# Optimization experiments

Hardware: AMD Instinct MI355X
Metric: run time of the kernel (lower is better)

The kernel has to match this reference:

```python
import jax, jax.numpy as jnp
import numpy as np

F = 26          # categorical fields
VOCAB = 10000   # per-field vocab
ED = 64         # embed_dim
NUM = 13        # numerical_num
B = 4096        # batch
E = 8           # expert_num
T = 2           # task_num
D = (F + 1) * ED            # embed_output_dim = 1728
BOT = [512, 256]
TOW = [128, 64]


def setup_inputs() -> dict:
    key = jax.random.key(0)
    ks = jax.random.split(key, 20)
    s = 0.02
    inp = {}
    inp['categorical_x'] = jax.random.randint(ks[0], (B, F), 0, VOCAB, dtype=jnp.int64 if jax.config.read('jax_enable_x64') else jnp.int32)
    inp['numerical_x'] = jax.random.normal(ks[1], (B, NUM), dtype=jnp.float32)
    # shared embedding table with per-field offsets (pytorch-fm EmbeddingLayer)
    inp['offsets'] = jnp.arange(F, dtype=jnp.int32) * VOCAB
    inp['W_emb'] = jax.random.normal(ks[2], (F * VOCAB, ED), dtype=jnp.float32) * s
    # numerical linear
    inp['Wn'] = jax.random.normal(ks[3], (NUM, ED), dtype=jnp.float32) * s
    inp['bn'] = jnp.zeros((ED,), dtype=jnp.float32)
    # experts (stacked): D -> 512 -> 256, ReLU after each (BN/dropout identity at eval)
    inp['We1'] = jax.random.normal(ks[4], (E, D, BOT[0]), dtype=jnp.float32) * s
    inp['be1'] = jnp.zeros((E, BOT[0]), dtype=jnp.float32)
    inp['We2'] = jax.random.normal(ks[5], (E, BOT[0], BOT[1]), dtype=jnp.float32) * s
    inp['be2'] = jnp.zeros((E, BOT[1]), dtype=jnp.float32)
    # gates: D -> E with softmax
    inp['Wg'] = jax.random.normal(ks[6], (T, D, E), dtype=jnp.float32) * s
    inp['bg'] = jnp.zeros((T, E), dtype=jnp.float32)
    # towers: 256 -> 128 -> 64 -> 1
    inp['Wt1'] = jax.random.normal(ks[7], (T, BOT[1], TOW[0]), dtype=jnp.float32) * s
    inp['bt1'] = jnp.zeros((T, TOW[0]), dtype=jnp.float32)
    inp['Wt2'] = jax.random.normal(ks[8], (T, TOW[0], TOW[1]), dtype=jnp.float32) * s
    inp['bt2'] = jnp.zeros((T, TOW[1]), dtype=jnp.float32)
    inp['Wt3'] = jax.random.normal(ks[9], (T, TOW[1], 1), dtype=jnp.float32) * s
    inp['bt3'] = jnp.zeros((T, 1), dtype=jnp.float32)
    return inp


def reference(categorical_x, numerical_x, offsets, W_emb, Wn, bn,
              We1, be1, We2, be2, Wg, bg,
              Wt1, bt1, Wt2, bt2, Wt3, bt3):
    b = categorical_x.shape[0]
    cat_emb = W_emb[categorical_x + offsets[None, :]]          # [B, F, ED]
    num_emb = numerical_x @ Wn + bn                            # [B, ED]
    emb = jnp.concatenate([cat_emb, num_emb[:, None, :]], axis=1).reshape(b, -1)  # [B, D]
    # all experts on the shared embedding (duplicate() gives identical copies per task)
    h = jax.nn.relu(jnp.einsum('bd,edh->ebh', emb, We1) + be1[:, None, :])        # [E, B, 512]
    fea = jax.nn.relu(jnp.einsum('ebh,eho->ebo', h, We2) + be2[:, None, :])       # [E, B, 256]
    # per-task softmax gating and weighted expert mixing
    gate = jax.nn.softmax(jnp.einsum('bd,tde->tbe', emb, Wg) + bg[:, None, :], axis=-1)  # [T, B, E]
    task_fea = jnp.einsum('tbe,ebo->tbo', gate, fea)                              # [T, B, 256]
    # towers
    h1 = jax.nn.relu(jnp.einsum('tbo,toh->tbh', task_fea, Wt1) + bt1[:, None, :])
    h2 = jax.nn.relu(jnp.einsum('tbh,thk->tbk', h1, Wt2) + bt2[:, None, :])
    logits = jnp.einsum('tbk,tko->tbo', h2, Wt3) + bt3[:, None, :]                # [T, B, 1]
    return jax.nn.sigmoid(logits[..., 0])                                         # [T, B]
```

## Files before the change

### kernel.cpp

```cpp
#include <hip/hip_runtime.h>
#include <hip/hip_bf16.h>

#define B_SZ 4096
#define F_CAT 26
#define NUM_N 13
#define ED 64
#define D_DIM 1728
#define E_EXP 8
#define T_TASK 2
#define BOT0 512
#define BOT1 256
#define TOW0 128
#define TOW1 64

typedef __bf16 bf16x8 __attribute__((ext_vector_type(8)));
typedef float f32x4 __attribute__((ext_vector_type(4)));
typedef float f32x16 __attribute__((ext_vector_type(16)));
typedef long lx2 __attribute__((ext_vector_type(2)));
typedef int i32x4 __attribute__((ext_vector_type(4)));
typedef int i32x8 __attribute__((ext_vector_type(8)));

#define SCL 0x7F7F7F7F

__device__ __forceinline__ void gload_lds16(const void* g, void* l) {
  __builtin_amdgcn_global_load_lds(
      (const __attribute__((address_space(1))) void*)g,
      (__attribute__((address_space(3))) void*)l, 16, 0, 0);
}

#define BAR() do { asm volatile("" ::: "memory"); __builtin_amdgcn_s_barrier(); asm volatile("" ::: "memory"); } while (0)
#define VM4() asm volatile("s_waitcnt vmcnt(4)" ::: "memory")
#define VM3() asm volatile("s_waitcnt vmcnt(3)" ::: "memory")

__device__ __forceinline__ int permk(int k6) {
  return (k6 & 7) + (((k6 >> 3) & 3) << 4) + (((k6 >> 5) & 1) << 3);
}

__device__ __forceinline__ size_t mxpos(int row, int kabs, int K) {
  int kt = kabs >> 6, kk = kabs & 63;
  int reg = row & ~63, ro = row & 63;
  int sub = ro >> 5, rr = ro & 31, r = rr & 15;
  int u = ((kk >> 5) << 1) | ((rr >> 4) & 1);
  int p = (kk >> 4) & 1;
  int g = (sub << 1) | p;
  return (size_t)(reg + g * 16 + r) * K + kt * 64 + u * 16 + (kk & 15);
}

__device__ __forceinline__ unsigned char f2e4m3_sw(float x) {
  unsigned su = (__float_as_uint(x) >> 24) & 0x80u;
  float ax = fabsf(x);
  if (!(ax < 448.f)) return (unsigned char)(su | 0x7E);
  if (ax == 0.f) return (unsigned char)su;
  int e;
  float m = frexpf(ax, &e);
  int E = e - 1;
  if (E < -6) {
    int mi = (int)rintf(ldexpf(ax, 9));
    if (mi >= 8) return (unsigned char)(su | 0x08);
    return (unsigned char)(su | mi);
  }
  int mi = (int)rintf(ldexpf(m, 4));
  if (mi == 16) { mi = 8; E += 1; if (E > 8) return (unsigned char)(su | 0x7E); }
  return (unsigned char)(su | ((E + 7) << 3) | (mi - 8));
}

#if __has_builtin(__builtin_amdgcn_cvt_pk_fp8_f32)
#define HAS_HW_FP8 1
__device__ __forceinline__ int cvtpk8_lo(float a, float b, int old) {
  return __builtin_amdgcn_cvt_pk_fp8_f32(a, b, old, false);
}
__device__ __forceinline__ int cvtpk8_hi(float a, float b, int old) {
  return __builtin_amdgcn_cvt_pk_fp8_f32(a, b, old, true);
}
__device__ __forceinline__ unsigned char f2e4m3(float x) {
  return (unsigned char)(__builtin_amdgcn_cvt_pk_fp8_f32(x, x, 0, false) & 0xFF);
}
#else
#define HAS_HW_FP8 0
__device__ __forceinline__ unsigned char f2e4m3(float x) { return f2e4m3_sw(x); }
#endif

__device__ __forceinline__ unsigned pk4_fp8(float a, float b, float c, float d) {
#if HAS_HW_FP8
  int v = cvtpk8_lo(a, b, 0);
  v = cvtpk8_hi(c, d, v);
  return (unsigned)v;
#else
  return (unsigned)f2e4m3_sw(a) | ((unsigned)f2e4m3_sw(b) << 8) |
         ((unsigned)f2e4m3_sw(c) << 16) | ((unsigned)f2e4m3_sw(d) << 24);
#endif
}

__device__ __forceinline__ void trans_tile_fp8mx(
    const float* __restrict__ inp, unsigned char* __restrict__ outp,
    int R, int C, int cx, int ry, float (*tile)[33])
{
  int c0 = cx * 32, r0 = ry * 32;
  int tx = threadIdx.x & 31, ty = threadIdx.x >> 5;
#pragma unroll
  for (int i = 0; i < 32; i += 8)
    tile[ty + i][tx] = inp[(size_t)(r0 + ty + i) * C + c0 + tx];
  __syncthreads();
  int ki = r0 + tx;
#pragma unroll
  for (int i = 0; i < 32; i += 8)
    outp[mxpos(c0 + ty + i, ki, R)] = f2e4m3(tile[tx][ty + i] * 16.f);
}

__global__ __launch_bounds__(256) void prep_weights(
    const float* __restrict__ We1, const float* __restrict__ We2,
    const float* __restrict__ Wg,
    unsigned char* __restrict__ We1T8, unsigned char* __restrict__ We2T8,
    unsigned char* __restrict__ WgT8)
{
  __shared__ float tile[32][33];
  int id = blockIdx.x;
  if (id < 6912) {
    int z = id / 864, r = id - z * 864;
    int cx = r & 15, ry = r >> 4;
    trans_tile_fp8mx(We1 + (size_t)z * D_DIM * BOT0, We1T8 + (size_t)z * D_DIM * BOT0,
                     D_DIM, BOT0, cx, ry, tile);
  } else if (id < 7936) {
    int r2 = id - 6912;
    int z = r2 >> 7, r = r2 & 127;
    int cx = r & 7, ry = r >> 3;
    trans_tile_fp8mx(We2 + (size_t)z * BOT0 * BOT1, We2T8 + (size_t)z * BOT0 * BOT1,
                     BOT0, BOT1, cx, ry, tile);
  } else {
    int i = (id - 7936) * 256 + threadIdx.x;
    int n = i / D_DIM, d = i - n * D_DIM;
    int t = n >> 3, e2 = n & 7;
    int pd = (d & ~63) + permk(d & 63);
    WgT8[(size_t)n * D_DIM + pd] =
        f2e4m3(Wg[((size_t)t * D_DIM + d) * E_EXP + e2] * 16.f);
  }
}

__global__ __launch_bounds__(256) void embed_convert(
    const int* __restrict__ cat, const float* __restrict__ numx,
    const int* __restrict__ offsets, const float* __restrict__ W_emb,
    const float* __restrict__ Wn, const float* __restrict__ bnum,
    unsigned char* __restrict__ emb8)
{
  int W = blockIdx.x * 256 + threadIdx.x;
  int prow = W / 108, ucol = W - prow * 108;
  int f = ucol >> 2, u = ucol & 3;
  int reg = prow & ~63, po = prow & 63;
  int g = po >> 4, r = po & 15;
  int sub = g >> 1, p = g & 1;
  int h = u >> 1, rbit = u & 1;
  int b = reg + sub * 32 + rbit * 16 + r;
  int kk = h * 32 + p * 16;
  float vals[16];
  if (f < F_CAT) {
    int row = cat[(size_t)b * F_CAT + f] + offsets[f];
    const float4* src = reinterpret_cast<const float4*>(&W_emb[(size_t)row * ED + kk]);
#pragma unroll
    for (int q = 0; q < 4; ++q) {
      float4 v = src[q];
      vals[q * 4 + 0] = v.x; vals[q * 4 + 1] = v.y;
      vals[q * 4 + 2] = v.z; vals[q * 4 + 3] = v.w;
    }
  } else {
#pragma unroll
    for (int j = 0; j < 16; ++j) vals[j] = bnum[kk + j];
    for (int n = 0; n < NUM_N; ++n) {
      float x = numx[(size_t)b * NUM_N + n];
      const float* wr = &Wn[n * ED + kk];
#pragma unroll
      for (int j = 0; j < 16; ++j) vals[j] = fmaf(x, wr[j], vals[j]);
    }
  }
  uint4 o;
  o.x = pk4_fp8(vals[0] * 16.f, vals[1] * 16.f, vals[2] * 16.f, vals[3] * 16.f);
  o.y = pk4_fp8(vals[4] * 16.f, vals[5] * 16.f, vals[6] * 16.f, vals[7] * 16.f);
  o.z = pk4_fp8(vals[8] * 16.f, vals[9] * 16.f, vals[10] * 16.f, vals[11] * 16.f);
  o.w = pk4_fp8(vals[12] * 16.f, vals[13] * 16.f, vals[14] * 16.f, vals[15] * 16.f);
  *reinterpret_cast<uint4*>(&emb8[(size_t)prow * D_DIM + f * 64 + u * 16]) = o;
}

__global__ __launch_bounds__(256) void gate_mfma(
    const unsigned char* __restrict__ emb8, const unsigned char* __restrict__ WgT8,
    const float* __restrict__ bg, float* __restrict__ gate)
{
  int wid = threadIdx.x >> 6, lane = threadIdx.x & 63;
  int l15 = lane & 15, lh = lane >> 4;
  int r0 = (blockIdx.x * 4 + wid) * 16;
  f32x4 acc = {};
  int b = r0 + l15;
  int reg = b & ~63, ro = b & 63;
  int sub = ro >> 5, rr = ro & 31;
  int rbit = (rr >> 4) & 1, rq = rr & 15;
  int pgh = lh >> 1;
  int prow = reg + (((sub << 1) | pgh) << 4) + rq;
  const unsigned char* arow = emb8 + (size_t)prow * D_DIM + rbit * 16 + (lh & 1) * 8;
  const unsigned char* brow = WgT8 + (size_t)l15 * D_DIM + lh * 16;
#pragma unroll 3
  for (int k = 0; k < D_DIM; k += 64) {
    long a0 = *reinterpret_cast<const long*>(arow + k);
    long a1 = *reinterpret_cast<const long*>(arow + k + 32);
    lx2 bv = *reinterpret_cast<const lx2*>(brow + k);
    acc = __builtin_amdgcn_mfma_f32_16x16x32_fp8_fp8(a0, bv[0], acc, 0, 0, 0);
    acc = __builtin_amdgcn_mfma_f32_16x16x32_fp8_fp8(a1, bv[1], acc, 0, 0, 0);
  }
  int t = l15 >> 3, e = l15 & 7;
  float bv = bg[t * E_EXP + e];
#pragma unroll
  for (int r = 0; r < 4; ++r) {
    float lg = acc[r] * (1.f / 256.f) + bv;
    float m = lg;
    m = fmaxf(m, __shfl_xor(m, 1));
    m = fmaxf(m, __shfl_xor(m, 2));
    m = fmaxf(m, __shfl_xor(m, 4));
    float ex = expf(lg - m);
    float s = ex;
    s += __shfl_xor(s, 1);
    s += __shfl_xor(s, 2);
    s += __shfl_xor(s, 4);
    int row = r0 + lh * 4 + r;
    gate[((size_t)t * B_SZ + row) * E_EXP + e] = ex / s;
  }
}

__device__ __forceinline__ i32x8 ld32(const char* base, int off) {
  i32x4 a = *reinterpret_cast<const i32x4*>(base + off);
  i32x4 b = *reinterpret_cast<const i32x4*>(base + off + 1024);
  i32x8 r;
  r[0] = a[0]; r[1] = a[1]; r[2] = a[2]; r[3] = a[3];
  r[4] = b[0]; r[5] = b[1]; r[6] = b[2]; r[7] = b[3];
  return r;
}

#define MXMFMA(va, vb, c) \
  __builtin_amdgcn_mfma_scale_f32_32x32x64_f8f6f4(va, vb, c, 0, 0, 0, SCL, 0, SCL)

__global__ __launch_bounds__(512, 2) void gemm_mx(
    const unsigned char* __restrict__ A8, size_t strideAe,
    const unsigned char* __restrict__ BT8,
    const float* __restrict__ bias,
    unsigned char* __restrict__ C8,
    int M, int N, int K)
{
  extern __shared__ char smem[];
  int e = blockIdx.z;
  const unsigned char* Ap = A8 + strideAe * (size_t)e;
  const unsigned char* Bp = BT8 + (size_t)e * N * K;
  const float* bp = bias + (size_t)e * N;
  unsigned char* Cp8 = C8 + (size_t)e * M * N;
  int bm0 = blockIdx.x * 256, bn0 = blockIdx.y * 256;

  int tid = threadIdx.x;
  int wid = tid >> 6, lane = tid & 63;
  int l15 = lane & 15, lh = lane >> 4;
  int l31 = lane & 31, hl = lane >> 5;
  int wrow = (wid >> 2) * 128, wcol = (wid & 3) * 64;

  int slotc = (lh ^ (((l15 >> 3) & 1) << 1)) << 4;
  const char* rdA = smem + (wrow + l15) * 64 + slotc;
  const char* rdB = smem + 49152 + (wcol + l15) * 64 + slotc;
  char* stA = smem + (wid << 10);
  char* stB = smem + 49152 + (wid << 10);

  int srow = tid >> 2;
  int ssw = (tid & 3) ^ (((srow >> 3) & 1) << 1);
  const unsigned char* gA0 = Ap + (size_t)(bm0 + srow) * K + ssw * 16;
  const unsigned char* gA1 = Ap + (size_t)(bm0 + 128 + srow) * K + ssw * 16;
  const unsigned char* gB0 = Bp + (size_t)(bn0 + srow) * K + ssw * 16;
  const unsigned char* gB1 = Bp + (size_t)(bn0 + 128 + srow) * K + ssw * 16;

  auto STAGE = [&](int koff, int buf) {
    gload_lds16(gA0 + koff, stA + buf * 16384);
    gload_lds16(gA1 + koff, stA + buf * 16384 + 8192);
    gload_lds16(gB0 + koff, stB + buf * 16384);
    gload_lds16(gB1 + koff, stB + buf * 16384 + 8192);
  };

  f32x16 acc[4][2] = {};
  int NT = K >> 6;

  STAGE(0, 0);
  STAGE(64, 1);
  VM4();
  BAR();

  int bufc = 0, koff = 128;
  for (int T = 0; T < NT; ++T) {
    const char* As = rdA + bufc * 16384;
    const char* Bs = rdB + bufc * 16384;
    int sb = bufc >= 1 ? bufc - 1 : 2;
    i32x8 va0, va1, vb0, vb1;

    va0 = ld32(As, 0);
    va1 = ld32(As, 2048);
    vb0 = ld32(Bs, 0);
    vb1 = ld32(Bs, 2048);
    STAGE(koff, sb);
    BAR();
    __builtin_amdgcn_s_setprio(1);
    acc[0][0] = MXMFMA(va0, vb0, acc[0][0]);
    acc[0][1] = MXMFMA(va0, vb1, acc[0][1]);
    acc[1][0] = MXMFMA(va1, vb0, acc[1][0]);
    acc[1][1] = MXMFMA(va1, vb1, acc[1][1]);
    __builtin_amdgcn_s_setprio(0);
    BAR();

    va0 = ld32(As, 4096);
    va1 = ld32(As, 4096 + 2048);
    BAR();
    __builtin_amdgcn_s_setprio(1);
    acc[2][0] = MXMFMA(va0, vb0, acc[2][0]);
    acc[2][1] = MXMFMA(va0, vb1, acc[2][1]);
    acc[3][0] = MXMFMA(va1, vb0, acc[3][0]);
    acc[3][1] = MXMFMA(va1, vb1, acc[3][1]);
    __builtin_amdgcn_s_setprio(0);
    VM4();
    BAR();

    koff += 64;
    bufc = bufc == 2 ? 0 : bufc + 1;
  }

  asm volatile("s_waitcnt vmcnt(0)" ::: "memory");
  BAR();
  unsigned char* cs8 = (unsigned char*)smem;
#pragma unroll
  for (int mi = 0; mi < 4; ++mi) {
#pragma unroll
    for (int nj = 0; nj < 2; ++nj) {
      int colT = wcol + nj * 32 + l31;
      float bv = bp[bn0 + colT];
      int kk = colT & 63;
      int ktrel = colT >> 6;
      int p = (kk >> 4) & 1;
      int ubase = (kk >> 5) << 1;
      int b4 = kk & 15;
      f32x16 a = acc[mi][nj];
      int rowBase = wrow + mi * 32 + (hl << 2);
#pragma unroll
      for (int rg = 0; rg < 16; rg += 2) {
        int row0 = rowBase + (rg & 3) + ((rg >> 2) << 3);
        float v0 = fmaxf(a[rg] * (1.f / 256.f) + bv, 0.f) * 16.f;
        float v1 = fmaxf(a[rg + 1] * (1.f / 256.f) + bv, 0.f) * 16.f;
#if HAS_HW_FP8
        int pk = cvtpk8_lo(v0, v1, 0);
#else
        int pk = (int)f2e4m3_sw(v0) | ((int)f2e4m3_sw(v1) << 8);
#endif
#pragma unroll
        for (int q = 0; q < 2; ++q) {
          int rowT = row0 + q;
          int regrel = rowT & ~63, ro = rowT & 63;
          int sub = ro >> 5, rr2 = ro & 31, r = rr2 & 15;
          int u = ubase | ((rr2 >> 4) & 1);
          int g = (sub << 1) | p;
          cs8[(regrel + g * 16 + r) * 256 + ktrel * 64 + u * 16 + b4] =
              (unsigned char)((pk >> (q * 8)) & 0xFF);
        }
      }
    }
  }
  BAR();
  {
    int rr = tid >> 4, c16 = (tid & 15) * 16;
#pragma unroll
    for (int p2 = 0; p2 < 8; ++p2) {
      int row = p2 * 32 + rr;
      *reinterpret_cast<uint4*>(&Cp8[(size_t)(bm0 + row) * N + bn0 + c16]) =
          *reinterpret_cast<const uint4*>(&cs8[(size_t)row * 256 + c16]);
    }
  }
}

__global__ __launch_bounds__(512, 2) void gemm_mx128(
    const unsigned char* __restrict__ A8, size_t strideAe,
    const unsigned char* __restrict__ BT8,
    const float* __restrict__ bias,
    __hip_bfloat16* __restrict__ C,
    int M, int N, int K)
{
  extern __shared__ char smem[];
  int e = blockIdx.z;
  const unsigned char* Ap = A8 + strideAe * (size_t)e;
  const unsigned char* Bp = BT8 + (size_t)e * N * K;
  const float* bp = bias + (size_t)e * N;
  __hip_bfloat16* Cp = C + (size_t)e * M * N;
  int bm0 = blockIdx.x * 128;

  int tid = threadIdx.x;
  int wid = tid >> 6, lane = tid & 63;
  int l15 = lane & 15, lh = lane >> 4;
  int l31 = lane & 31, hl = lane >> 5;
  int wrow = (wid >> 2) * 64, wcol = (wid & 3) * 64;

  int slotc = (lh ^ (((l15 >> 3) & 1) << 1)) << 4;
  const char* rdA = smem + (wrow + l15) * 64 + slotc;
  const char* rdB = smem + 24576 + (wcol + l15) * 64 + slotc;
  char* stA = smem + (wid << 10);
  char* stB = smem + 24576 + (wid << 10);

  int srow = tid >> 2;
  int ssw = (tid & 3) ^ (((srow >> 3) & 1) << 1);
  const unsigned char* gA0 = Ap + (size_t)(bm0 + srow) * K + ssw * 16;
  const unsigned char* gB0 = Bp + (size_t)srow * K + ssw * 16;
  const unsigned char* gB1 = Bp + (size_t)(128 + srow) * K + ssw * 16;

  auto STAGE = [&](int koff, int buf) {
    gload_lds16(gA0 + koff, stA + buf * 8192);
    gload_lds16(gB0 + koff, stB + buf * 16384);
    gload_lds16(gB1 + koff, stB + buf * 16384 + 8192);
  };

  f32x16 acc[2][2] = {};
  int NT = K >> 6;

  STAGE(0, 0);
  STAGE(64, 1);
  VM3();
  BAR();

  int bufc = 0, koff = 128;
  for (int T = 0; T < NT; ++T) {
    const char* As = rdA + bufc * 8192;
    const char* Bs = rdB + bufc * 16384;
    int sb = bufc >= 1 ? bufc - 1 : 2;
    i32x8 va, vb0, vb1;

    va = ld32(As, 0);
    vb0 = ld32(Bs, 0);
    vb1 = ld32(Bs, 2048);
    STAGE(koff, sb);
    BAR();
    __builtin_amdgcn_s_setprio(1);
    acc[0][0] = MXMFMA(va, vb0, acc[0][0]);
    acc[0][1] = MXMFMA(va, vb1, acc[0][1]);
    __builtin_amdgcn_s_setprio(0);
    BAR();

    va = ld32(As, 2048);
    BAR();
    __builtin_amdgcn_s_setprio(1);
    acc[1][0] = MXMFMA(va, vb0, acc[1][0]);
    acc[1][1] = MXMFMA(va, vb1, acc[1][1]);
    __builtin_amdgcn_s_setprio(0);
    VM3();
    BAR();

    koff += 64;
    bufc = bufc == 2 ? 0 : bufc + 1;
  }

  asm volatile("s_waitcnt vmcnt(0)" ::: "memory");
  BAR();
  __hip_bfloat16* cs = (__hip_bfloat16*)smem;
#pragma unroll
  for (int mi = 0; mi < 2; ++mi) {
#pragma unroll
    for (int nj = 0; nj < 2; ++nj) {
      int colT = wcol + nj * 32 + l31;
      float bv = bp[colT];
      f32x16 a = acc[mi][nj];
#pragma unroll
      for (int rg = 0; rg < 16; ++rg) {
        int rowT = wrow + mi * 32 + (rg & 3) + ((rg >> 2) << 3) + (hl << 2);
        float v = a[rg] * (1.f / 256.f) + bv;
        cs[(size_t)rowT * 256 + colT] = __float2bfloat16(fmaxf(v, 0.f));
      }
    }
  }
  BAR();
  {
    int rr = tid >> 5, c8 = (tid & 31) * 8;
#pragma unroll
    for (int p2 = 0; p2 < 8; ++p2) {
      int row = p2 * 16 + rr;
      *reinterpret_cast<uint4*>(&Cp[(size_t)(bm0 + row) * N + c8]) =
          *reinterpret_cast<const uint4*>(&cs[(size_t)row * 256 + c8]);
    }
  }
}

#define TB 16
__global__ __launch_bounds__(256) void combine_tower(
    const float* __restrict__ gate, const __hip_bfloat16* __restrict__ fea,
    const float* __restrict__ Wt1, const float* __restrict__ bt1,
    const float* __restrict__ Wt2, const float* __restrict__ bt2,
    const float* __restrict__ Wt3, const float* __restrict__ bt3,
    float* __restrict__ out)
{
  int t = blockIdx.y;
  int b0 = blockIdx.x * TB;
  int tid = threadIdx.x;
  __shared__ float gs[TB][E_EXP];
  __shared__ float tf[TB][BOT1];
  __shared__ float h1[TB][TOW0];
  __shared__ float h2[TB][TOW1];
  if (tid < TB * E_EXP) {
    int bl = tid >> 3, e = tid & 7;
    gs[bl][e] = gate[((size_t)t * B_SZ + b0 + bl) * E_EXP + e];
  }
  __syncthreads();
  for (int i = tid; i < TB * BOT1; i += 256) {
    int bl = i >> 8, o = i & 255;
    float s = 0.f;
#pragma unroll
    for (int e = 0; e < E_EXP; ++e)
      s = fmaf(gs[bl][e], __bfloat162float(fea[((size_t)e * B_SZ + b0 + bl) * BOT1 + o]), s);
    tf[bl][o] = s;
  }
  __syncthreads();
  {
    int h = tid & 127, half = tid >> 7;
    float a[8] = {0, 0, 0, 0, 0, 0, 0, 0};
    for (int d = 0; d < BOT1; ++d) {
      float w = Wt1[((size_t)t * BOT1 + d) * TOW0 + h];
#pragma unroll
      for (int q = 0; q < 8; ++q) a[q] = fmaf(w, tf[half * 8 + q][d], a[q]);
    }
    float bv = bt1[t * TOW0 + h];
#pragma unroll
    for (int q = 0; q < 8; ++q) h1[half * 8 + q][h] = fmaxf(a[q] + bv, 0.f);
  }
  __syncthreads();
  {
    int h = tid & 63, qt = tid >> 6;
    float a[4] = {0, 0, 0, 0};
    for (int d = 0; d < TOW0; ++d) {
      float w = Wt2[((size_t)t * TOW0 + d) * TOW1 + h];
#pragma unroll
      for (int q = 0; q < 4; ++q) a[q] = fmaf(w, h1[qt * 4 + q][d], a[q]);
    }
    float bv = bt2[t * TOW1 + h];
#pragma unroll
    for (int q = 0; q < 4; ++q) h2[qt * 4 + q][h] = fmaxf(a[q] + bv, 0.f);
  }
  __syncthreads();
  {
    int l16 = tid & 15, bl = tid >> 4;
    float p = 0.f;
#pragma unroll
    for (int d = l16; d < TOW1; d += 16) p = fmaf(h2[bl][d], Wt3[t * TOW1 + d], p);
#pragma unroll
    for (int o = 8; o; o >>= 1) p += __shfl_down(p, o, 16);
    if (l16 == 0) {
      float lg = p + bt3[t];
      out[(size_t)t * B_SZ + b0 + bl] = 1.f / (1.f + expf(-lg));
    }
  }
}

extern "C" void kernel_launch(void* const* d_in, const int* in_sizes, int n_in,
                              void* d_out, int out_size, void* d_ws, size_t ws_size,
                              hipStream_t stream) {
  const int* cat = (const int*)d_in[0];
  const float* numx = (const float*)d_in[1];
  const int* offsets = (const int*)d_in[2];
  const float* W_emb = (const float*)d_in[3];
  const float* Wn = (const float*)d_in[4];
  const float* bnv = (const float*)d_in[5];
  const float* We1 = (const float*)d_in[6];
  const float* be1 = (const float*)d_in[7];
  const float* We2 = (const float*)d_in[8];
  const float* be2 = (const float*)d_in[9];
  const float* Wg = (const float*)d_in[10];
  const float* bg = (const float*)d_in[11];
  const float* Wt1 = (const float*)d_in[12];
  const float* bt1 = (const float*)d_in[13];
  const float* Wt2 = (const float*)d_in[14];
  const float* bt2 = (const float*)d_in[15];
  const float* Wt3 = (const float*)d_in[16];
  const float* bt3 = (const float*)d_in[17];
  float* out = (float*)d_out;

  char* ws = (char*)d_ws;
  size_t off = 0;
  auto alloc = [&](size_t bytes) {
    char* p = ws + off;
    off += (bytes + 255) & ~(size_t)255;
    return p;
  };
  unsigned char*  emb8  = (unsigned char*)alloc((size_t)B_SZ * D_DIM);
  unsigned char*  We1T8 = (unsigned char*)alloc((size_t)E_EXP * BOT0 * D_DIM);
  unsigned char*  We2T8 = (unsigned char*)alloc((size_t)E_EXP * BOT1 * BOT0);
  unsigned char*  H8    = (unsigned char*)alloc((size_t)E_EXP * B_SZ * BOT0);
  __hip_bfloat16* fea   = (__hip_bfloat16*)alloc((size_t)E_EXP * B_SZ * BOT1 * 2);
  float* gate = (float*)alloc((size_t)T_TASK * B_SZ * E_EXP * 4);
  unsigned char*  WgT8  = (unsigned char*)alloc((size_t)T_TASK * E_EXP * D_DIM);
  (void)alloc(4096);

  hipFuncSetAttribute((const void*)gemm_mx,
                      hipFuncAttributeMaxDynamicSharedMemorySize, 98304);
  hipFuncSetAttribute((const void*)gemm_mx128,
                      hipFuncAttributeMaxDynamicSharedMemorySize, 73728);

  prep_weights<<<dim3(8044), 256, 0, stream>>>(We1, We2, Wg, We1T8, We2T8, WgT8);

  embed_convert<<<dim3(B_SZ * 108 / 256), 256, 0, stream>>>(
      cat, numx, offsets, W_emb, Wn, bnv, emb8);

  gate_mfma<<<dim3(B_SZ / 64), 256, 0, stream>>>(emb8, WgT8, bg, gate);

  gemm_mx<<<dim3(B_SZ / 256, BOT0 / 256, E_EXP), 512, 98304, stream>>>(
      emb8, (size_t)0, We1T8, be1, H8, B_SZ, BOT0, D_DIM);

  gemm_mx128<<<dim3(B_SZ / 128, 1, E_EXP), 512, 73728, stream>>>(
      H8, (size_t)B_SZ * BOT0, We2T8, be2, fea, B_SZ, BOT1, BOT0);

  combine_tower<<<dim3(B_SZ / TB, T_TASK), 256, 0, stream>>>(
      gate, fea, Wt1, bt1, Wt2, bt2, Wt3, bt3, out);
}
```

Measured before the change: 105.1 us.

## Store expert features as fp8 and merge weight prep with embedding conversion

The second expert GEMM now writes its ReLU output as scaled fp8 e4m3 instead of bf16. This halves the fea buffer traffic between gemm_mx128 and combine_tower, and the tower decodes it with a software dec8 and folds the 1/16 scale into the gate weights. The weight-prep and embedding-conversion kernels are merged into one launch to save a kernel boundary. The cost is lower precision in the expert features and extra decode ALU work in combine_tower.

```diff
diff --git a/kernel.cpp b/kernel.cpp
--- a/kernel.cpp
+++ b/kernel.cpp
@@ -91,6 +91,13 @@
 #endif
 }
 
+__device__ __forceinline__ float dec8(unsigned char v) {
+  int e = (v >> 3) & 15, m = v & 7;
+  float mag = e ? __int_as_float(((e + 120) << 23) | (m << 20))
+                : (float)m * 0.001953125f;
+  return (v & 0x80) ? -mag : mag;
+}
+
 __device__ __forceinline__ void trans_tile_fp8mx(
     const float* __restrict__ inp, unsigned char* __restrict__ outp,
     int R, int C, int cx, int ry, float (*tile)[33])
@@ -107,11 +114,14 @@
     outp[mxpos(c0 + ty + i, ki, R)] = f2e4m3(tile[tx][ty + i] * 16.f);
 }
 
-__global__ __launch_bounds__(256) void prep_weights(
+__global__ __launch_bounds__(256) void prep_all(
     const float* __restrict__ We1, const float* __restrict__ We2,
     const float* __restrict__ Wg,
+    const int* __restrict__ cat, const float* __restrict__ numx,
+    const int* __restrict__ offsets, const float* __restrict__ W_emb,
+    const float* __restrict__ Wn, const float* __restrict__ bnum,
     unsigned char* __restrict__ We1T8, unsigned char* __restrict__ We2T8,
-    unsigned char* __restrict__ WgT8)
+    unsigned char* __restrict__ WgT8, unsigned char* __restrict__ emb8)
 {
   __shared__ float tile[32][33];
   int id = blockIdx.x;
@@ -126,57 +136,50 @@
     int cx = r & 7, ry = r >> 3;
     trans_tile_fp8mx(We2 + (size_t)z * BOT0 * BOT1, We2T8 + (size_t)z * BOT0 * BOT1,
                      BOT0, BOT1, cx, ry, tile);
-  } else {
+  } else if (id < 8044) {
     int i = (id - 7936) * 256 + threadIdx.x;
     int n = i / D_DIM, d = i - n * D_DIM;
     int t = n >> 3, e2 = n & 7;
     int pd = (d & ~63) + permk(d & 63);
     WgT8[(size_t)n * D_DIM + pd] =
         f2e4m3(Wg[((size_t)t * D_DIM + d) * E_EXP + e2] * 16.f);
-  }
-}
-
-__global__ __launch_bounds__(256) void embed_convert(
-    const int* __restrict__ cat, const float* __restrict__ numx,
-    const int* __restrict__ offsets, const float* __restrict__ W_emb,
-    const float* __restrict__ Wn, const float* __restrict__ bnum,
-    unsigned char* __restrict__ emb8)
-{
-  int W = blockIdx.x * 256 + threadIdx.x;
-  int prow = W / 108, ucol = W - prow * 108;
-  int f = ucol >> 2, u = ucol & 3;
-  int reg = prow & ~63, po = prow & 63;
-  int g = po >> 4, r = po & 15;
-  int sub = g >> 1, p = g & 1;
-  int h = u >> 1, rbit = u & 1;
-  int b = reg + sub * 32 + rbit * 16 + r;
-  int kk = h * 32 + p * 16;
-  float vals[16];
-  if (f < F_CAT) {
-    int row = cat[(size_t)b * F_CAT + f] + offsets[f];
-    const float4* src = reinterpret_cast<const float4*>(&W_emb[(size_t)row * ED + kk]);
-#pragma unroll
-    for (int q = 0; q < 4; ++q) {
-      float4 v = src[q];
-      vals[q * 4 + 0] = v.x; vals[q * 4 + 1] = v.y;
-      vals[q * 4 + 2] = v.z; vals[q * 4 + 3] = v.w;
-    }
   } else {
-#pragma unroll
-    for (int j = 0; j < 16; ++j) vals[j] = bnum[kk + j];
-    for (int n = 0; n < NUM_N; ++n) {
-      float x = numx[(size_t)b * NUM_N + n];
-      const float* wr = &Wn[n * ED + kk];
-#pragma unroll
-      for (int j = 0; j < 16; ++j) vals[j] = fmaf(x, wr[j], vals[j]);
-    }
-  }
-  uint4 o;
-  o.x = pk4_fp8(vals[0] * 16.f, vals[1] * 16.f, vals[2] * 16.f, vals[3] * 16.f);
-  o.y = pk4_fp8(vals[4] * 16.f, vals[5] * 16.f, vals[6] * 16.f, vals[7] * 16.f);
-  o.z = pk4_fp8(vals[8] * 16.f, vals[9] * 16.f, vals[10] * 16.f, vals[11] * 16.f);
-  o.w = pk4_fp8(vals[12] * 16.f, vals[13] * 16.f, vals[14] * 16.f, vals[15] * 16.f);
-  *reinterpret_cast<uint4*>(&emb8[(size_t)prow * D_DIM + f * 64 + u * 16]) = o;
+    int W = (id - 8044) * 256 + threadIdx.x;
+    int prow = W / 108, ucol = W - prow * 108;
+    int f = ucol >> 2, u = ucol & 3;
+    int reg = prow & ~63, po = prow & 63;
+    int g = po >> 4, r = po & 15;
+    int sub = g >> 1, p = g & 1;
+    int h = u >> 1, rbit = u & 1;
+    int b = reg + sub * 32 + rbit * 16 + r;
+    int kk = h * 32 + p * 16;
+    float vals[16];
+    if (f < F_CAT) {
+      int row = cat[(size_t)b * F_CAT + f] + offsets[f];
+      const float4* src = reinterpret_cast<const float4*>(&W_emb[(size_t)row * ED + kk]);
+#pragma unroll
+      for (int q = 0; q < 4; ++q) {
+        float4 v = src[q];
+        vals[q * 4 + 0] = v.x; vals[q * 4 + 1] = v.y;
+        vals[q * 4 + 2] = v.z; vals[q * 4 + 3] = v.w;
+      }
+    } else {
+#pragma unroll
+      for (int j = 0; j < 16; ++j) vals[j] = bnum[kk + j];
+      for (int n = 0; n < NUM_N; ++n) {
+        float x = numx[(size_t)b * NUM_N + n];
+        const float* wr = &Wn[n * ED + kk];
+#pragma unroll
+        for (int j = 0; j < 16; ++j) vals[j] = fmaf(x, wr[j], vals[j]);
+      }
+    }
+    uint4 o;
+    o.x = pk4_fp8(vals[0] * 16.f, vals[1] * 16.f, vals[2] * 16.f, vals[3] * 16.f);
+    o.y = pk4_fp8(vals[4] * 16.f, vals[5] * 16.f, vals[6] * 16.f, vals[7] * 16.f);
+    o.z = pk4_fp8(vals[8] * 16.f, vals[9] * 16.f, vals[10] * 16.f, vals[11] * 16.f);
+    o.w = pk4_fp8(vals[12] * 16.f, vals[13] * 16.f, vals[14] * 16.f, vals[15] * 16.f);
+    *reinterpret_cast<uint4*>(&emb8[(size_t)prow * D_DIM + f * 64 + u * 16]) = o;
+  }
 }
 
 __global__ __launch_bounds__(256) void gate_mfma(
@@ -375,7 +378,7 @@
     const unsigned char* __restrict__ A8, size_t strideAe,
     const unsigned char* __restrict__ BT8,
     const float* __restrict__ bias,
-    __hip_bfloat16* __restrict__ C,
+    unsigned char* __restrict__ C8,
     int M, int N, int K)
 {
   extern __shared__ char smem[];
@@ -383,7 +386,7 @@
   const unsigned char* Ap = A8 + strideAe * (size_t)e;
   const unsigned char* Bp = BT8 + (size_t)e * N * K;
   const float* bp = bias + (size_t)e * N;
-  __hip_bfloat16* Cp = C + (size_t)e * M * N;
+  unsigned char* Cp8 = C8 + (size_t)e * M * N;
   int bm0 = blockIdx.x * 128;
 
   int tid = threadIdx.x;
@@ -451,7 +454,7 @@
 
   asm volatile("s_waitcnt vmcnt(0)" ::: "memory");
   BAR();
-  __hip_bfloat16* cs = (__hip_bfloat16*)smem;
+  unsigned char* cs8 = (unsigned char*)smem;
 #pragma unroll
   for (int mi = 0; mi < 2; ++mi) {
 #pragma unroll
@@ -459,29 +462,37 @@
       int colT = wcol + nj * 32 + l31;
       float bv = bp[colT];
       f32x16 a = acc[mi][nj];
-#pragma unroll
-      for (int rg = 0; rg < 16; ++rg) {
-        int rowT = wrow + mi * 32 + (rg & 3) + ((rg >> 2) << 3) + (hl << 2);
-        float v = a[rg] * (1.f / 256.f) + bv;
-        cs[(size_t)rowT * 256 + colT] = __float2bfloat16(fmaxf(v, 0.f));
+      int rowBase = wrow + mi * 32 + (hl << 2);
+#pragma unroll
+      for (int rg = 0; rg < 16; rg += 2) {
+        int row0 = rowBase + (rg & 3) + ((rg >> 2) << 3);
+        float v0 = fmaxf(a[rg] * (1.f / 256.f) + bv, 0.f) * 16.f;
+        float v1 = fmaxf(a[rg + 1] * (1.f / 256.f) + bv, 0.f) * 16.f;
+#if HAS_HW_FP8
+        int pk = cvtpk8_lo(v0, v1, 0);
+#else
+        int pk = (int)f2e4m3_sw(v0) | ((int)f2e4m3_sw(v1) << 8);
+#endif
+        cs8[(size_t)row0 * 256 + colT] = (unsigned char)(pk & 0xFF);
+        cs8[(size_t)(row0 + 1) * 256 + colT] = (unsigned char)((pk >> 8) & 0xFF);
       }
     }
   }
   BAR();
   {
-    int rr = tid >> 5, c8 = (tid & 31) * 8;
-#pragma unroll
-    for (int p2 = 0; p2 < 8; ++p2) {
-      int row = p2 * 16 + rr;
-      *reinterpret_cast<uint4*>(&Cp[(size_t)(bm0 + row) * N + c8]) =
-          *reinterpret_cast<const uint4*>(&cs[(size_t)row * 256 + c8]);
+    int rr = tid >> 4, c16 = (tid & 15) * 16;
+#pragma unroll
+    for (int p2 = 0; p2 < 4; ++p2) {
+      int row = p2 * 32 + rr;
+      *reinterpret_cast<uint4*>(&Cp8[(size_t)(bm0 + row) * N + c16]) =
+          *reinterpret_cast<const uint4*>(&cs8[(size_t)row * 256 + c16]);
     }
   }
 }
 
 #define TB 16
 __global__ __launch_bounds__(256) void combine_tower(
-    const float* __restrict__ gate, const __hip_bfloat16* __restrict__ fea,
+    const float* __restrict__ gate, const unsigned char* __restrict__ fea8,
     const float* __restrict__ Wt1, const float* __restrict__ bt1,
     const float* __restrict__ Wt2, const float* __restrict__ bt2,
     const float* __restrict__ Wt3, const float* __restrict__ bt3,
@@ -496,7 +507,7 @@
   __shared__ float h2[TB][TOW1];
   if (tid < TB * E_EXP) {
     int bl = tid >> 3, e = tid & 7;
-    gs[bl][e] = gate[((size_t)t * B_SZ + b0 + bl) * E_EXP + e];
+    gs[bl][e] = gate[((size_t)t * B_SZ + b0 + bl) * E_EXP + e] * (1.f / 16.f);
   }
   __syncthreads();
   for (int i = tid; i < TB * BOT1; i += 256) {
@@ -504,7 +515,8 @@
     float s = 0.f;
 #pragma unroll
     for (int e = 0; e < E_EXP; ++e)
-      s = fmaf(gs[bl][e], __bfloat162float(fea[((size_t)e * B_SZ + b0 + bl) * BOT1 + o]), s);
+      s = fmaf(gs[bl][e],
+               dec8(fea8[((size_t)e * B_SZ + b0 + bl) * BOT1 + o]), s);
     tf[bl][o] = s;
   }
   __syncthreads();
@@ -582,7 +594,7 @@
   unsigned char*  We1T8 = (unsigned char*)alloc((size_t)E_EXP * BOT0 * D_DIM);
   unsigned char*  We2T8 = (unsigned char*)alloc((size_t)E_EXP * BOT1 * BOT0);
   unsigned char*  H8    = (unsigned char*)alloc((size_t)E_EXP * B_SZ * BOT0);
-  __hip_bfloat16* fea   = (__hip_bfloat16*)alloc((size_t)E_EXP * B_SZ * BOT1 * 2);
+  unsigned char*  fea8  = (unsigned char*)alloc((size_t)E_EXP * B_SZ * BOT1);
   float* gate = (float*)alloc((size_t)T_TASK * B_SZ * E_EXP * 4);
   unsigned char*  WgT8  = (unsigned char*)alloc((size_t)T_TASK * E_EXP * D_DIM);
   (void)alloc(4096);
@@ -592,10 +604,9 @@
   hipFuncSetAttribute((const void*)gemm_mx128,
                       hipFuncAttributeMaxDynamicSharedMemorySize, 73728);
 
-  prep_weights<<<dim3(8044), 256, 0, stream>>>(We1, We2, Wg, We1T8, We2T8, WgT8);
-
-  embed_convert<<<dim3(B_SZ * 108 / 256), 256, 0, stream>>>(
-      cat, numx, offsets, W_emb, Wn, bnv, emb8);
+  prep_all<<<dim3(8044 + B_SZ * 108 / 256), 256, 0, stream>>>(
+      We1, We2, Wg, cat, numx, offsets, W_emb, Wn, bnv,
+      We1T8, We2T8, WgT8, emb8);
 
   gate_mfma<<<dim3(B_SZ / 64), 256, 0, stream>>>(emb8, WgT8, bg, gate);
 
@@ -603,8 +614,8 @@
       emb8, (size_t)0, We1T8, be1, H8, B_SZ, BOT0, D_DIM);
 
   gemm_mx128<<<dim3(B_SZ / 128, 1, E_EXP), 512, 73728, stream>>>(
-      H8, (size_t)B_SZ * BOT0, We2T8, be2, fea, B_SZ, BOT1, BOT0);
+      H8, (size_t)B_SZ * BOT0, We2T8, be2, fea8, B_SZ, BOT1, BOT0);
 
   combine_tower<<<dim3(B_SZ / TB, T_TASK), 256, 0, stream>>>(
-      gate, fea, Wt1, bt1, Wt2, bt2, Wt3, bt3, out);
-}
+      gate, fea8, Wt1, bt1, Wt2, bt2, Wt3, bt3, out);
+}
```

Measured after the change: 106.4 us. No clear change (+1.2%).

## Quantize first expert GEMM operands to FP4 (e2m1) MX format

Applied to the files above, without the earlier changes.

Converts the embedding and the first expert weight matrix to packed FP4 (e2m1) with a new interleaved layout. The first expert GEMM then runs FP4 scaled MFMAs, which halves the operand bytes per K step and raises MFMA throughput. The embed kernel now writes both an FP8 and an FP4 copy of the embedding. This greatly reduces numerical precision (only 8 magnitude levels) and risks failing accuracy tolerance. The loop restructuring, with a tail iteration for K=1728 as 13.5 128-wide steps, adds complexity.

```diff
diff --git a/kernel.cpp b/kernel.cpp
--- a/kernel.cpp
+++ b/kernel.cpp
@@ -6,6 +6,7 @@
 #define NUM_N 13
 #define ED 64
 #define D_DIM 1728
+#define KS4 896
 #define E_EXP 8
 #define T_TASK 2
 #define BOT0 512
@@ -44,6 +45,17 @@
   int p = (kk >> 4) & 1;
   int g = (sub << 1) | p;
   return (size_t)(reg + g * 16 + r) * K + kt * 64 + u * 16 + (kk & 15);
+}
+
+__device__ __forceinline__ size_t mx4pos(int row, int k, int stride) {
+  int kt = k >> 7, kr = k & 127;
+  int j = kr >> 6, kk = kr & 63;
+  int hb = (kk >> 5) & 1, b = (kk & 31) >> 1;
+  int reg = row & ~63, ro = row & 63;
+  int sub = ro >> 5, rr = ro & 31, rbit = (rr >> 4) & 1, rq = rr & 15;
+  int g = (sub << 1) | j;
+  int u = (hb << 1) | rbit;
+  return (size_t)(reg + g * 16 + rq) * stride + kt * 64 + u * 16 + b;
 }
 
 __device__ __forceinline__ unsigned char f2e4m3_sw(float x) {
@@ -91,6 +103,21 @@
 #endif
 }
 
+__device__ __forceinline__ unsigned f2e2m1(float x) {
+  unsigned s = x < 0.f ? 8u : 0u;
+  float a = fabsf(x);
+  unsigned m;
+  if (a < 0.25f) m = 0;
+  else if (a < 0.75f) m = 1;
+  else if (a < 1.25f) m = 2;
+  else if (a < 1.75f) m = 3;
+  else if (a < 2.5f)  m = 4;
+  else if (a < 3.5f)  m = 5;
+  else if (a < 5.f)   m = 6;
+  else m = 7;
+  return s | m;
+}
+
 __device__ __forceinline__ void trans_tile_fp8mx(
     const float* __restrict__ inp, unsigned char* __restrict__ outp,
     int R, int C, int cx, int ry, float (*tile)[33])
@@ -107,10 +134,29 @@
     outp[mxpos(c0 + ty + i, ki, R)] = f2e4m3(tile[tx][ty + i] * 16.f);
 }
 
+__device__ __forceinline__ void trans_tile_fp4(
+    const float* __restrict__ inp, unsigned char* __restrict__ outp,
+    int C, int cx, int ry, float (*tile)[33])
+{
+  int c0 = cx * 32, r0 = ry * 32;
+  int tx = threadIdx.x & 31, ty = threadIdx.x >> 5;
+#pragma unroll
+  for (int i = 0; i < 32; i += 8)
+    tile[ty + i][tx] = inp[(size_t)(r0 + ty + i) * C + c0 + tx];
+  __syncthreads();
+#pragma unroll
+  for (int w = threadIdx.x; w < 512; w += 256) {
+    int nl = w & 31, bp = w >> 5;
+    unsigned by = f2e2m1(tile[2 * bp][nl] * 64.f) |
+                  (f2e2m1(tile[2 * bp + 1][nl] * 64.f) << 4);
+    outp[mx4pos(c0 + nl, r0 + 2 * bp, KS4)] = (unsigned char)by;
+  }
+}
+
 __global__ __launch_bounds__(256) void prep_weights(
     const float* __restrict__ We1, const float* __restrict__ We2,
     const float* __restrict__ Wg,
-    unsigned char* __restrict__ We1T8, unsigned char* __restrict__ We2T8,
+    unsigned char* __restrict__ We1T4, unsigned char* __restrict__ We2T8,
     unsigned char* __restrict__ WgT8)
 {
   __shared__ float tile[32][33];
@@ -118,8 +164,8 @@
   if (id < 6912) {
     int z = id / 864, r = id - z * 864;
     int cx = r & 15, ry = r >> 4;
-    trans_tile_fp8mx(We1 + (size_t)z * D_DIM * BOT0, We1T8 + (size_t)z * D_DIM * BOT0,
-                     D_DIM, BOT0, cx, ry, tile);
+    trans_tile_fp4(We1 + (size_t)z * D_DIM * BOT0, We1T4 + (size_t)z * BOT0 * KS4,
+                   BOT0, cx, ry, tile);
   } else if (id < 7936) {
     int r2 = id - 6912;
     int z = r2 >> 7, r = r2 & 127;
@@ -140,7 +186,7 @@
     const int* __restrict__ cat, const float* __restrict__ numx,
     const int* __restrict__ offsets, const float* __restrict__ W_emb,
     const float* __restrict__ Wn, const float* __restrict__ bnum,
-    unsigned char* __restrict__ emb8)
+    unsigned char* __restrict__ emb8, unsigned char* __restrict__ emb4)
 {
   int W = blockIdx.x * 256 + threadIdx.x;
   int prow = W / 108, ucol = W - prow * 108;
@@ -177,6 +223,16 @@
   o.z = pk4_fp8(vals[8] * 16.f, vals[9] * 16.f, vals[10] * 16.f, vals[11] * 16.f);
   o.w = pk4_fp8(vals[12] * 16.f, vals[13] * 16.f, vals[14] * 16.f, vals[15] * 16.f);
   *reinterpret_cast<uint4*>(&emb8[(size_t)prow * D_DIM + f * 64 + u * 16]) = o;
+
+  unsigned long long pk8 = 0;
+#pragma unroll
+  for (int c = 0; c < 8; ++c) {
+    unsigned by = f2e2m1(vals[2 * c] * 32.f) |
+                  (f2e2m1(vals[2 * c + 1] * 32.f) << 4);
+    pk8 |= (unsigned long long)by << (8 * c);
+  }
+  int k0g = f * 64 + kk;
+  *reinterpret_cast<unsigned long long*>(&emb4[mx4pos(b, k0g, KS4)]) = pk8;
 }
 
 __global__ __launch_bounds__(256) void gate_mfma(
@@ -231,20 +287,28 @@
   return r;
 }
 
+__device__ __forceinline__ i32x8 hi8(i32x8 v) {
+  i32x8 r = v;
+  r[0] = v[4]; r[1] = v[5]; r[2] = v[6]; r[3] = v[7];
+  return r;
+}
+
 #define MXMFMA(va, vb, c) \
   __builtin_amdgcn_mfma_scale_f32_32x32x64_f8f6f4(va, vb, c, 0, 0, 0, SCL, 0, SCL)
-
-__global__ __launch_bounds__(512, 2) void gemm_mx(
-    const unsigned char* __restrict__ A8, size_t strideAe,
-    const unsigned char* __restrict__ BT8,
+#define MX4MFMA(va, vb, c) \
+  __builtin_amdgcn_mfma_scale_f32_32x32x64_f8f6f4(va, vb, c, 4, 4, 0, SCL, 0, SCL)
+
+__global__ __launch_bounds__(512, 2) void gemm_mx4(
+    const unsigned char* __restrict__ A4, size_t strideAe,
+    const unsigned char* __restrict__ BT4,
     const float* __restrict__ bias,
     unsigned char* __restrict__ C8,
     int M, int N, int K)
 {
   extern __shared__ char smem[];
   int e = blockIdx.z;
-  const unsigned char* Ap = A8 + strideAe * (size_t)e;
-  const unsigned char* Bp = BT8 + (size_t)e * N * K;
+  const unsigned char* Ap = A4 + strideAe * (size_t)e;
+  const unsigned char* Bp = BT4 + (size_t)e * N * KS4;
   const float* bp = bias + (size_t)e * N;
   unsigned char* Cp8 = C8 + (size_t)e * M * N;
   int bm0 = blockIdx.x * 256, bn0 = blockIdx.y * 256;
@@ -263,10 +327,10 @@
 
   int srow = tid >> 2;
   int ssw = (tid & 3) ^ (((srow >> 3) & 1) << 1);
-  const unsigned char* gA0 = Ap + (size_t)(bm0 + srow) * K + ssw * 16;
-  const unsigned char* gA1 = Ap + (size_t)(bm0 + 128 + srow) * K + ssw * 16;
-  const unsigned char* gB0 = Bp + (size_t)(bn0 + srow) * K + ssw * 16;
-  const unsigned char* gB1 = Bp + (size_t)(bn0 + 128 + srow) * K + ssw * 16;
+  const unsigned char* gA0 = Ap + (size_t)(bm0 + srow) * KS4 + ssw * 16;
+  const unsigned char* gA1 = Ap + (size_t)(bm0 + 128 + srow) * KS4 + ssw * 16;
+  const unsigned char* gB0 = Bp + (size_t)(bn0 + srow) * KS4 + ssw * 16;
+  const unsigned char* gB1 = Bp + (size_t)(bn0 + 128 + srow) * KS4 + ssw * 16;
 
   auto STAGE = [&](int koff, int buf) {
     gload_lds16(gA0 + koff, stA + buf * 16384);
@@ -276,7 +340,7 @@
   };
 
   f32x16 acc[4][2] = {};
-  int NT = K >> 6;
+  int NTf = K >> 7;
 
   STAGE(0, 0);
   STAGE(64, 1);
@@ -284,7 +348,7 @@
   BAR();
 
   int bufc = 0, koff = 128;
-  for (int T = 0; T < NT; ++T) {
+  for (int T = 0; T < NTf; ++T) {
     const char* As = rdA + bufc * 16384;
     const char* Bs = rdB + bufc * 16384;
     int sb = bufc >= 1 ? bufc - 1 : 2;
@@ -297,27 +361,47 @@
     STAGE(koff, sb);
     BAR();
     __builtin_amdgcn_s_setprio(1);
-    acc[0][0] = MXMFMA(va0, vb0, acc[0][0]);
-    acc[0][1] = MXMFMA(va0, vb1, acc[0][1]);
-    acc[1][0] = MXMFMA(va1, vb0, acc[1][0]);
-    acc[1][1] = MXMFMA(va1, vb1, acc[1][1]);
+    acc[0][0] = MX4MFMA(va0, vb0, acc[0][0]);
+    acc[0][0] = MX4MFMA(hi8(va0), hi8(vb0), acc[0][0]);
+    acc[0][1] = MX4MFMA(va0, vb1, acc[0][1]);
+    acc[0][1] = MX4MFMA(hi8(va0), hi8(vb1), acc[0][1]);
+    acc[1][0] = MX4MFMA(va1, vb0, acc[1][0]);
+    acc[1][0] = MX4MFMA(hi8(va1), hi8(vb0), acc[1][0]);
+    acc[1][1] = MX4MFMA(va1, vb1, acc[1][1]);
+    acc[1][1] = MX4MFMA(hi8(va1), hi8(vb1), acc[1][1]);
     __builtin_amdgcn_s_setprio(0);
     BAR();
 
     va0 = ld32(As, 4096);
-    va1 = ld32(As, 4096 + 2048);
+    va1 = ld32(As, 6144);
     BAR();
     __builtin_amdgcn_s_setprio(1);
-    acc[2][0] = MXMFMA(va0, vb0, acc[2][0]);
-    acc[2][1] = MXMFMA(va0, vb1, acc[2][1]);
-    acc[3][0] = MXMFMA(va1, vb0, acc[3][0]);
-    acc[3][1] = MXMFMA(va1, vb1, acc[3][1]);
+    acc[2][0] = MX4MFMA(va0, vb0, acc[2][0]);
+    acc[2][0] = MX4MFMA(hi8(va0), hi8(vb0), acc[2][0]);
+    acc[2][1] = MX4MFMA(va0, vb1, acc[2][1]);
+    acc[2][1] = MX4MFMA(hi8(va0), hi8(vb1), acc[2][1]);
+    acc[3][0] = MX4MFMA(va1, vb0, acc[3][0]);
+    acc[3][0] = MX4MFMA(hi8(va1), hi8(vb0), acc[3][0]);
+    acc[3][1] = MX4MFMA(va1, vb1, acc[3][1]);
+    acc[3][1] = MX4MFMA(hi8(va1), hi8(vb1), acc[3][1]);
     __builtin_amdgcn_s_setprio(0);
     VM4();
     BAR();
 
     koff += 64;
     bufc = bufc == 2 ? 0 : bufc + 1;
+  }
+
+  {
+    const char* As = rdA + bufc * 16384;
+    const char* Bs = rdB + bufc * 16384;
+    i32x8 vb0 = ld32(Bs, 0), vb1 = ld32(Bs, 2048);
+#pragma unroll
+    for (int mi = 0; mi < 4; ++mi) {
+      i32x8 va = ld32(As, mi * 2048);
+      acc[mi][0] = MX4MFMA(va, vb0, acc[mi][0]);
+      acc[mi][1] = MX4MFMA(va, vb1, acc[mi][1]);
+    }
   }
 
   asm volatile("s_waitcnt vmcnt(0)" ::: "memory");
@@ -339,8 +423,8 @@
 #pragma unroll
       for (int rg = 0; rg < 16; rg += 2) {
         int row0 = rowBase + (rg & 3) + ((rg >> 2) << 3);
-        float v0 = fmaxf(a[rg] * (1.f / 256.f) + bv, 0.f) * 16.f;
-        float v1 = fmaxf(a[rg + 1] * (1.f / 256.f) + bv, 0.f) * 16.f;
+        float v0 = fmaxf(a[rg] * (1.f / 2048.f) + bv, 0.f) * 16.f;
+        float v1 = fmaxf(a[rg + 1] * (1.f / 2048.f) + bv, 0.f) * 16.f;
 #if HAS_HW_FP8
         int pk = cvtpk8_lo(v0, v1, 0);
 #else
@@ -579,28 +663,29 @@
     return p;
   };
   unsigned char*  emb8  = (unsigned char*)alloc((size_t)B_SZ * D_DIM);
-  unsigned char*  We1T8 = (unsigned char*)alloc((size_t)E_EXP * BOT0 * D_DIM);
+  unsigned char*  emb4  = (unsigned char*)alloc((size_t)B_SZ * KS4);
+  unsigned char*  We1T4 = (unsigned char*)alloc((size_t)E_EXP * BOT0 * KS4);
   unsigned char*  We2T8 = (unsigned char*)alloc((size_t)E_EXP * BOT1 * BOT0);
   unsigned char*  H8    = (unsigned char*)alloc((size_t)E_EXP * B_SZ * BOT0);
   __hip_bfloat16* fea   = (__hip_bfloat16*)alloc((size_t)E_EXP * B_SZ * BOT1 * 2);
   float* gate = (float*)alloc((size_t)T_TASK * B_SZ * E_EXP * 4);
   unsigned char*  WgT8  = (unsigned char*)alloc((size_t)T_TASK * E_EXP * D_DIM);
-  (void)alloc(4096);
-
-  hipFuncSetAttribute((const void*)gemm_mx,
+  (void)alloc(8192);
+
+  hipFuncSetAttribute((const void*)gemm_mx4,
                       hipFuncAttributeMaxDynamicSharedMemorySize, 98304);
   hipFuncSetAttribute((const void*)gemm_mx128,
                       hipFuncAttributeMaxDynamicSharedMemorySize, 73728);
 
-  prep_weights<<<dim3(8044), 256, 0, stream>>>(We1, We2, Wg, We1T8, We2T8, WgT8);
+  prep_weights<<<dim3(8044), 256, 0, stream>>>(We1, We2, Wg, We1T4, We2T8, WgT8);
 
   embed_convert<<<dim3(B_SZ * 108 / 256), 256, 0, stream>>>(
-      cat, numx, offsets, W_emb, Wn, bnv, emb8);
+      cat, numx, offsets, W_emb, Wn, bnv, emb8, emb4);
 
   gate_mfma<<<dim3(B_SZ / 64), 256, 0, stream>>>(emb8, WgT8, bg, gate);
 
-  gemm_mx<<<dim3(B_SZ / 256, BOT0 / 256, E_EXP), 512, 98304, stream>>>(
-      emb8, (size_t)0, We1T8, be1, H8, B_SZ, BOT0, D_DIM);
+  gemm_mx4<<<dim3(B_SZ / 256, BOT0 / 256, E_EXP), 512, 98304, stream>>>(
+      emb4, (size_t)0, We1T4, be1, H8, B_SZ, BOT0, D_DIM);
 
   gemm_mx128<<<dim3(B_SZ / 128, 1, E_EXP), 512, 73728, stream>>>(
       H8, (size_t)B_SZ * BOT0, We2T8, be2, fea, B_SZ, BOT1, BOT0);
```

New measurement: 101.0 us. 4.0% less time.
